# Kernel tuning notes

Hardware: AMD Instinct MI355X
Metric: run time of the kernel (lower is better)

## Reference

```python
import jax, jax.numpy as jnp
import numpy as np

N = 100_000      # nodes
E = 800_000      # edges
NF = 32          # node_feature_size
EF = 32          # edge_feature_size
L = 64           # layer_size
ENTRY = NF + EF          # 64, input width of node_mlp_1
SECOND = NF + L          # 96, input width of node_mlp_2
SLOPE = 0.1              # leakiness
EPS = 1e-5               # BatchNorm1d eps


def _bn(h, g, b):
    # BatchNorm1d in training mode: batch mean, biased variance
    m = h.mean(0)
    v = ((h - m) ** 2).mean(0)
    return (h - m) * jax.lax.rsqrt(v + EPS) * g + b


def _lrelu(h):
    return jnp.where(h > 0, h, SLOPE * h)


def setup_inputs() -> dict:
    key = jax.random.key(0)
    ks = jax.random.split(key, 16)

    def w(k, i, o):
        return (jax.random.normal(k, (i, o), jnp.float32) / np.float32(np.sqrt(i)))

    def bvec(k, o):
        return jax.random.normal(k, (o,), jnp.float32) * 0.01

    inp = {
        "x": jax.random.normal(ks[0], (N, NF), jnp.float32),
        "edge_index": jax.random.randint(ks[1], (2, E), 0, N),
        "edge_attr": jax.random.normal(ks[2], (E, EF), jnp.float32),
        "u": jax.random.normal(ks[3], (1, 4), jnp.float32),
        "batch": jnp.zeros((N,), jnp.int32),
        # node_mlp_1 params
        "m1_g1": jnp.ones((ENTRY,), jnp.float32), "m1_b1": jnp.zeros((ENTRY,), jnp.float32),
        "m1_w1": w(ks[4], ENTRY, L), "m1_c1": bvec(ks[5], L),
        "m1_g2": jnp.ones((L,), jnp.float32), "m1_b2": jnp.zeros((L,), jnp.float32),
        "m1_w2": w(ks[6], L, L), "m1_c2": bvec(ks[7], L),
        "m1_g3": jnp.ones((L,), jnp.float32), "m1_b3": jnp.zeros((L,), jnp.float32),
        "m1_w3": w(ks[8], L, L), "m1_c3": bvec(ks[9], L),
        # node_mlp_2 params
        "m2_g1": jnp.ones((SECOND,), jnp.float32), "m2_b1": jnp.zeros((SECOND,), jnp.float32),
        "m2_w1": w(ks[10], SECOND, SECOND), "m2_c1": bvec(ks[11], SECOND),
        "m2_g2": jnp.ones((SECOND,), jnp.float32), "m2_b2": jnp.zeros((SECOND,), jnp.float32),
        "m2_w2": w(ks[12], SECOND, SECOND), "m2_c2": bvec(ks[13], SECOND),
        "m2_g3": jnp.ones((SECOND,), jnp.float32), "m2_b3": jnp.zeros((SECOND,), jnp.float32),
        "m2_w3": w(ks[14], SECOND, NF), "m2_c3": bvec(ks[15], NF),
    }
    return inp


def reference(x, edge_index, edge_attr, u, batch,
              m1_g1, m1_b1, m1_w1, m1_c1,
              m1_g2, m1_b2, m1_w2, m1_c2,
              m1_g3, m1_b3, m1_w3, m1_c3,
              m2_g1, m2_b1, m2_w1, m2_c1,
              m2_g2, m2_b2, m2_w2, m2_c2,
              m2_g3, m2_b3, m2_w3, m2_c3):
    row, col = edge_index[0], edge_index[1]
    # gather source node features, concat with edge features  [E, ENTRY]
    h = jnp.concatenate([x[row], edge_attr], axis=1)
    # node_mlp_1: BN -> Linear -> LReLU -> BN -> Linear -> LReLU -> BN -> Linear
    h = _lrelu(_bn(h, m1_g1, m1_b1) @ m1_w1 + m1_c1)
    h = _lrelu(_bn(h, m1_g2, m1_b2) @ m1_w2 + m1_c2)
    h = _bn(h, m1_g3, m1_b3) @ m1_w3 + m1_c3
    # scatter-sum back to destination nodes  [N, L]
    agg = jax.ops.segment_sum(h, col, num_segments=x.shape[0])
    # node_mlp_2 on [x, agg]  [N, SECOND]
    h2 = jnp.concatenate([x, agg], axis=1)
    h2 = _lrelu(_bn(h2, m2_g1, m2_b1) @ m2_w1 + m2_c1)
    h2 = _lrelu(_bn(h2, m2_g2, m2_b2) @ m2_w2 + m2_c2)
    out = _bn(h2, m2_g3, m2_b3) @ m2_w3 + m2_c3  # [N, NF]
    return out
```

## Files before the change

kernel.cpp:

```cpp
#include <hip/hip_runtime.h>


typedef unsigned short u16;
typedef __bf16  bf16x8  __attribute__((ext_vector_type(8)));
typedef float   floatx4 __attribute__((ext_vector_type(4)));

#define NBIN 8

__device__ __forceinline__ float bf2f(u16 u) {
  union { float f; unsigned int i; } v; v.i = ((unsigned int)u) << 16; return v.f;
}
__device__ __forceinline__ u16 f2bf(float f) {
  union { float f; unsigned int i; } v; v.f = f;
  unsigned int x = v.i;
  return (u16)((x + 0x7fffu + ((x >> 16) & 1u)) >> 16);
}
__device__ __forceinline__ bf16x8 ldb8(const u16* p) {
  return *reinterpret_cast<const bf16x8*>(p);
}
__device__ __forceinline__ floatx4 mfma16(bf16x8 a, bf16x8 b, floatx4 c) {
  return __builtin_amdgcn_mfma_f32_16x16x32_bf16(a, b, c, 0, 0, 0);
}
__device__ __forceinline__ float loadf(const void* p, long idx, int mode) {
  return mode ? bf2f(((const u16*)p)[idx]) : ((const float*)p)[idx];
}
__device__ __forceinline__ bf16x8 load8(const void* p, long idx, int mode) {
  if (mode) return ldb8((const u16*)p + idx);
  const float* f = (const float*)p + idx;
  bf16x8 r;
#pragma unroll
  for (int j = 0; j < 8; j++) r[j] = (__bf16)f[j];
  return r;
}

__global__ void detect_kernel(const u16* __restrict__ x, int* __restrict__ modep) {
  __shared__ int cnt;
  if (threadIdx.x == 0) cnt = 0;
  __syncthreads();
  int weird = 0;
  for (int i = threadIdx.x; i < 1024; i += blockDim.x) {
    unsigned e = (x[i] >> 7) & 0xFFu;
    if (e == 0xFFu || e >= 0x90u || (e != 0u && e < 0x60u)) weird++;
  }
  atomicAdd(&cnt, weird);
  __syncthreads();
  if (threadIdx.x == 0) *modep = (cnt > 128) ? 0 : 1;
}

__global__ void count_kernel(const int* __restrict__ col, int E,
                             int* __restrict__ deg) {
  for (int e = blockIdx.x * blockDim.x + threadIdx.x; e < E;
       e += gridDim.x * blockDim.x)
    atomicAdd(&deg[col[e]], 1);
}

__global__ void scan1_kernel(const int* __restrict__ deg, int n,
                             int* __restrict__ excl, int* __restrict__ bsum) {
  __shared__ int tmp[2][1024];
  const int tid = threadIdx.x;
  const int i = blockIdx.x * 1024 + tid;
  int v = (i < n) ? deg[i] : 0;
  tmp[0][tid] = v;
  __syncthreads();
  int src = 0;
  for (int off = 1; off < 1024; off <<= 1) {
    int t = tmp[src][tid];
    if (tid >= off) t += tmp[src][tid - off];
    tmp[1 - src][tid] = t;
    src = 1 - src;
    __syncthreads();
  }
  if (i < n) excl[i] = tmp[src][tid] - v;
  if (tid == 1023) bsum[blockIdx.x] = tmp[src][1023];
}

__global__ void scan2_kernel(int* __restrict__ bsum, int nb,
                             int* __restrict__ offsets, int N, int E) {
  if (threadIdx.x == 0) {
    int run = 0;
    for (int i = 0; i < nb; i++) { int v = bsum[i]; bsum[i] = run; run += v; }
    offsets[N] = E;
  }
}

__global__ void scan3_kernel(int* __restrict__ offsets, const int* __restrict__ bsum,
                             int n, int* __restrict__ cursor) {
  int i = blockIdx.x * 1024 + threadIdx.x;
  if (i < n) {
    int v = offsets[i] + bsum[blockIdx.x];
    offsets[i] = v;
    cursor[i] = v;
  }
}

__global__ void scatter_kernel(const int* __restrict__ col, int E,
                               int* __restrict__ cursor, int* __restrict__ perm) {
  for (int e = blockIdx.x * blockDim.x + threadIdx.x; e < E;
       e += gridDim.x * blockDim.x) {
    int d = col[e];
    int pos = atomicAdd(&cursor[d], 1);
    perm[pos] = e;
  }
}

__global__ __launch_bounds__(256) void aggsum_kernel(
    const u16* __restrict__ h_e, const int* __restrict__ perm,
    const int* __restrict__ offsets, float* __restrict__ s_e, int N) {
  const int lane = threadIdx.x & 63, wave = threadIdx.x >> 6;
  for (long n = (long)blockIdx.x * 4 + wave; n < N; n += (long)gridDim.x * 4) {
    int start = offsets[n], end = offsets[n + 1];
    float acc = 0.f;
    for (int j = start; j < end; j++) {
      long e = perm[j];
      acc += bf2f(h_e[e * 64 + lane]);
    }
    s_e[n * 64 + lane] = acc;
  }
}

__global__ void stats0_kernel(const void* __restrict__ x, const void* __restrict__ ea,
                              const int* __restrict__ erow, int E,
                              float* __restrict__ stats, const int* __restrict__ modep) {
  const int mode = *modep;
  const int c = threadIdx.x & 63, es = threadIdx.x >> 6;
  float s = 0.f, q = 0.f;
  for (long e = (long)blockIdx.x * 4 + es; e < E; e += (long)gridDim.x * 4) {
    float v;
    if (c < 32) { int src = erow[e]; v = loadf(x, (long)src * 32 + c, mode); }
    else        { v = loadf(ea, e * 32 + (c - 32), mode); }
    s += v; q += v * v;
  }
  __shared__ float sm1[256], sm2[256];
  sm1[threadIdx.x] = s; sm2[threadIdx.x] = q;
  __syncthreads();
  if (es == 0) {
    for (int i = 1; i < 4; i++) { s += sm1[i * 64 + c]; q += sm2[i * 64 + c]; }
    float* o = stats + (blockIdx.x & (NBIN - 1)) * 128;
    atomicAdd(o + c, s); atomicAdd(o + 64 + c, q);
  }
}

__global__ void statsX_kernel(const void* __restrict__ x, int N,
                              float* __restrict__ stats,
                              const int* __restrict__ modep) {
  const int mode = *modep;
  const int c = threadIdx.x & 31, rs = threadIdx.x >> 5;
  float s = 0.f, q = 0.f;
  for (long r = (long)blockIdx.x * 8 + rs; r < N; r += (long)gridDim.x * 8) {
    float v = loadf(x, r * 32 + c, mode);
    s += v; q += v * v;
  }
  __shared__ float sm1[256], sm2[256];
  sm1[threadIdx.x] = s; sm2[threadIdx.x] = q;
  __syncthreads();
  if (rs == 0) {
    for (int i = 1; i < 8; i++) { s += sm1[i * 32 + c]; q += sm2[i * 32 + c]; }
    float* o = stats + (blockIdx.x & (NBIN - 1)) * 192;
    atomicAdd(o + c, s); atomicAdd(o + 96 + c, q);
  }
}

__global__ void fold_kernel(const float* __restrict__ stats, float inv_rows,
                            const void* __restrict__ g, const void* __restrict__ b,
                            const void* __restrict__ W, const void* __restrict__ c,
                            int K, int OUT,
                            u16* __restrict__ Wpack, float* __restrict__ biasOut,
                            const int* __restrict__ modep) {
  const int mode = *modep;
  __shared__ float s_s[96], s_off[96];
  const int tid = threadIdx.x;
  if (tid < K) {
    float sum = 0.f, sq = 0.f;
    for (int p = 0; p < NBIN; p++) {
      sum += stats[p * 2 * K + tid];
      sq  += stats[p * 2 * K + K + tid];
    }
    float m   = sum * inv_rows;
    float var = sq * inv_rows - m * m;
    float s   = loadf(g, tid, mode) * rsqrtf(var + 1e-5f);
    s_s[tid]  = s;
    s_off[tid] = loadf(b, tid, mode) - m * s;
  }
  __syncthreads();
  for (int n = tid; n < OUT; n += blockDim.x) {
    float acc = loadf(c, n, mode);
    for (int k = 0; k < K; k++) acc += s_off[k] * loadf(W, k * OUT + n, mode);
    biasOut[n] = acc;
  }
  const int H = K / 32, T = OUT / 16;
  const int total = T * H * 64 * 8;
  for (int i = tid; i < total; i += blockDim.x) {
    int j = i & 7, lane = (i >> 3) & 63, th = i >> 9;
    int h = th % H, t = th / H;
    int k = h * 32 + (lane >> 4) * 8 + j;
    int n = t * 16 + (lane & 15);
    Wpack[i] = f2bf(s_s[k] * loadf(W, k * OUT + n, mode));
  }
}


__global__ __launch_bounds__(256) void gemm1_kernel(
    const void* __restrict__ x, const void* __restrict__ ea,
    const int* __restrict__ erow, const u16* __restrict__ Wp,
    const float* __restrict__ bias, u16* __restrict__ hout, int E,
    float* __restrict__ statsOut, const int* __restrict__ modep) {
  const int mode = *modep;
  const int lane = threadIdx.x & 63, wave = threadIdx.x >> 6;
  const int q = lane >> 4, r = lane & 15;
  const long wbase = (long)blockIdx.x * 256 + wave * 64;
  bf16x8 bfr[4][2];
#pragma unroll
  for (int t = 0; t < 4; t++)
#pragma unroll
    for (int h = 0; h < 2; h++)
      bfr[t][h] = ldb8(Wp + ((t * 2 + h) * 64 + lane) * 8);
  float bv[4];
#pragma unroll
  for (int t = 0; t < 4; t++) bv[t] = bias[t * 16 + r];
  float s_[4] = {0, 0, 0, 0}, q_[4] = {0, 0, 0, 0};
#pragma unroll
  for (int r4 = 0; r4 < 4; r4++) {
    const long row0 = wbase + r4 * 16;
    long e = row0 + r; if (e > E - 1) e = E - 1;
    int src = erow[e];
    bf16x8 a0 = load8(x, (long)src * 32 + q * 8, mode);
    bf16x8 a1 = load8(ea, e * 32 + q * 8, mode);
    floatx4 acc[4];
#pragma unroll
    for (int t = 0; t < 4; t++) {
      acc[t] = (floatx4){bv[t], bv[t], bv[t], bv[t]};
      acc[t] = mfma16(a0, bfr[t][0], acc[t]);
      acc[t] = mfma16(a1, bfr[t][1], acc[t]);
    }
#pragma unroll
    for (int t = 0; t < 4; t++)
#pragma unroll
      for (int gi = 0; gi < 4; gi++) {
        long row = row0 + q * 4 + gi;
        if (row < E) {
          float v = acc[t][gi];
          v = v > 0.f ? v : 0.1f * v;
          u16 st = f2bf(v);
          hout[row * 64 + t * 16 + r] = st;
          float vv = bf2f(st);
          s_[t] += vv; q_[t] += vv * vv;
        }
      }
  }
  __shared__ float sm[512];
#pragma unroll
  for (int t = 0; t < 4; t++) {
    float s = s_[t], qq = q_[t];
    s  += __shfl_xor(s, 16, 64);  s  += __shfl_xor(s, 32, 64);
    qq += __shfl_xor(qq, 16, 64); qq += __shfl_xor(qq, 32, 64);
    if (lane < 16) { sm[wave * 128 + t * 16 + lane] = s; sm[wave * 128 + 64 + t * 16 + lane] = qq; }
  }
  __syncthreads();
  if (threadIdx.x < 128) {
    int which = threadIdx.x >> 6, c = threadIdx.x & 63;
    float v = 0.f;
    for (int w = 0; w < 4; w++) v += sm[w * 128 + which * 64 + c];
    atomicAdd(statsOut + (blockIdx.x & (NBIN - 1)) * 128 + which * 64 + c, v);
  }
}

__global__ __launch_bounds__(256) void gemm2_kernel(
    const u16* __restrict__ hin, const u16* __restrict__ Wp,
    const float* __restrict__ bias, u16* __restrict__ hout, int E,
    float* __restrict__ statsOut) {
  const int lane = threadIdx.x & 63, wave = threadIdx.x >> 6;
  const int q = lane >> 4, r = lane & 15;
  const long wbase = (long)blockIdx.x * 256 + wave * 64;
  bf16x8 bfr[4][2];
#pragma unroll
  for (int t = 0; t < 4; t++)
#pragma unroll
    for (int h = 0; h < 2; h++)
      bfr[t][h] = ldb8(Wp + ((t * 2 + h) * 64 + lane) * 8);
  float bv[4];
#pragma unroll
  for (int t = 0; t < 4; t++) bv[t] = bias[t * 16 + r];
  float s_[4] = {0, 0, 0, 0}, q_[4] = {0, 0, 0, 0};
#pragma unroll
  for (int r4 = 0; r4 < 4; r4++) {
    const long row0 = wbase + r4 * 16;
    long e = row0 + r; if (e > E - 1) e = E - 1;
    bf16x8 a0 = ldb8(hin + e * 64 + q * 8);
    bf16x8 a1 = ldb8(hin + e * 64 + 32 + q * 8);
    floatx4 acc[4];
#pragma unroll
    for (int t = 0; t < 4; t++) {
      acc[t] = (floatx4){bv[t], bv[t], bv[t], bv[t]};
      acc[t] = mfma16(a0, bfr[t][0], acc[t]);
      acc[t] = mfma16(a1, bfr[t][1], acc[t]);
    }
#pragma unroll
    for (int t = 0; t < 4; t++)
#pragma unroll
      for (int gi = 0; gi < 4; gi++) {
        long row = row0 + q * 4 + gi;
        if (row < E) {
          float v = acc[t][gi];
          v = v > 0.f ? v : 0.1f * v;
          u16 st = f2bf(v);
          hout[row * 64 + t * 16 + r] = st;
          float vv = bf2f(st);
          s_[t] += vv; q_[t] += vv * vv;
        }
      }
  }
  __shared__ float sm[512];
#pragma unroll
  for (int t = 0; t < 4; t++) {
    float s = s_[t], qq = q_[t];
    s  += __shfl_xor(s, 16, 64);  s  += __shfl_xor(s, 32, 64);
    qq += __shfl_xor(qq, 16, 64); qq += __shfl_xor(qq, 32, 64);
    if (lane < 16) { sm[wave * 128 + t * 16 + lane] = s; sm[wave * 128 + 64 + t * 16 + lane] = qq; }
  }
  __syncthreads();
  if (threadIdx.x < 128) {
    int which = threadIdx.x >> 6, c = threadIdx.x & 63;
    float v = 0.f;
    for (int w = 0; w < 4; w++) v += sm[w * 128 + which * 64 + c];
    atomicAdd(statsOut + (blockIdx.x & (NBIN - 1)) * 128 + which * 64 + c, v);
  }
}

__global__ __launch_bounds__(256) void gemmAgg_kernel(
    const float* __restrict__ s_e, const int* __restrict__ deg,
    const u16* __restrict__ Wp, const float* __restrict__ bias,
    float* __restrict__ agg, int N, float* __restrict__ statsOut) {
  const int lane = threadIdx.x & 63, wave = threadIdx.x >> 6;
  const int q = lane >> 4, r = lane & 15;
  const long wbase = (long)blockIdx.x * 256 + wave * 64;
  bf16x8 bfr[4][2];
#pragma unroll
  for (int t = 0; t < 4; t++)
#pragma unroll
    for (int h = 0; h < 2; h++)
      bfr[t][h] = ldb8(Wp + ((t * 2 + h) * 64 + lane) * 8);
  float bv[4];
#pragma unroll
  for (int t = 0; t < 4; t++) bv[t] = bias[t * 16 + r];
  float s_[4] = {0, 0, 0, 0}, q_[4] = {0, 0, 0, 0};
#pragma unroll
  for (int r4 = 0; r4 < 4; r4++) {
    const long row0 = wbase + r4 * 16;
    long m = row0 + r;
    long mm = m < N ? m : (long)N - 1;
    bf16x8 a0, a1;
    {
      const float* ap = s_e + mm * 64 + q * 8;
#pragma unroll
      for (int j = 0; j < 8; j++) a0[j] = (__bf16)ap[j];
#pragma unroll
      for (int j = 0; j < 8; j++) a1[j] = (__bf16)ap[32 + j];
    }
    floatx4 acc[4];
#pragma unroll
    for (int t = 0; t < 4; t++) {
      acc[t] = (floatx4){0.f, 0.f, 0.f, 0.f};
      acc[t] = mfma16(a0, bfr[t][0], acc[t]);
      acc[t] = mfma16(a1, bfr[t][1], acc[t]);
    }
#pragma unroll
    for (int gi = 0; gi < 4; gi++) {
      long row = row0 + q * 4 + gi;
      if (row < N) {
        float d = (float)deg[row];
#pragma unroll
        for (int t = 0; t < 4; t++) {
          float v = acc[t][gi] + d * bv[t];
          agg[row * 64 + t * 16 + r] = v;
          s_[t] += v; q_[t] += v * v;
        }
      }
    }
  }
  __shared__ float sm[512];
#pragma unroll
  for (int t = 0; t < 4; t++) {
    float s = s_[t], qq = q_[t];
    s  += __shfl_xor(s, 16, 64);  s  += __shfl_xor(s, 32, 64);
    qq += __shfl_xor(qq, 16, 64); qq += __shfl_xor(qq, 32, 64);
    if (lane < 16) { sm[wave * 128 + t * 16 + lane] = s; sm[wave * 128 + 64 + t * 16 + lane] = qq; }
  }
  __syncthreads();
  if (threadIdx.x < 128) {
    int which = threadIdx.x >> 6, c = threadIdx.x & 63;
    float v = 0.f;
    for (int w = 0; w < 4; w++) v += sm[w * 128 + which * 64 + c];
    atomicAdd(statsOut + (blockIdx.x & (NBIN - 1)) * 192 + which * 96 + 32 + c, v);
  }
}


__global__ __launch_bounds__(256) void gemmB1_kernel(
    const void* __restrict__ x, const float* __restrict__ agg,
    const u16* __restrict__ Wp, const float* __restrict__ bias,
    u16* __restrict__ hout, int N, float* __restrict__ statsOut,
    const int* __restrict__ modep) {
  const int mode = *modep;
  const int lane = threadIdx.x & 63, wave = threadIdx.x >> 6;
  const int q = lane >> 4, r = lane & 15;
  const long wbase = (long)blockIdx.x * 256 + wave * 64;
  bf16x8 bfr[6][3];
#pragma unroll
  for (int t = 0; t < 6; t++)
#pragma unroll
    for (int h = 0; h < 3; h++)
      bfr[t][h] = ldb8(Wp + ((t * 3 + h) * 64 + lane) * 8);
  float bv[6];
#pragma unroll
  for (int t = 0; t < 6; t++) bv[t] = bias[t * 16 + r];
  float s_[6] = {0, 0, 0, 0, 0, 0}, q_[6] = {0, 0, 0, 0, 0, 0};
#pragma unroll
  for (int r4 = 0; r4 < 4; r4++) {
    const long row0 = wbase + r4 * 16;
    long m = row0 + r;
    long mm = m < N ? m : (long)N - 1;
    bf16x8 a0 = load8(x, mm * 32 + q * 8, mode);
    bf16x8 a1, a2;
    {
      const float* ap = agg + mm * 64 + q * 8;
#pragma unroll
      for (int j = 0; j < 8; j++) a1[j] = (__bf16)ap[j];
#pragma unroll
      for (int j = 0; j < 8; j++) a2[j] = (__bf16)ap[32 + j];
    }
    floatx4 acc[6];
#pragma unroll
    for (int t = 0; t < 6; t++) {
      acc[t] = (floatx4){bv[t], bv[t], bv[t], bv[t]};
      acc[t] = mfma16(a0, bfr[t][0], acc[t]);
      acc[t] = mfma16(a1, bfr[t][1], acc[t]);
      acc[t] = mfma16(a2, bfr[t][2], acc[t]);
    }
#pragma unroll
    for (int t = 0; t < 6; t++)
#pragma unroll
      for (int gi = 0; gi < 4; gi++) {
        long row = row0 + q * 4 + gi;
        if (row < N) {
          float v = acc[t][gi];
          v = v > 0.f ? v : 0.1f * v;
          u16 st = f2bf(v);
          hout[row * 96 + t * 16 + r] = st;
          float vv = bf2f(st);
          s_[t] += vv; q_[t] += vv * vv;
        }
      }
  }
  __shared__ float sm[768];
#pragma unroll
  for (int t = 0; t < 6; t++) {
    float s = s_[t], qq = q_[t];
    s  += __shfl_xor(s, 16, 64);  s  += __shfl_xor(s, 32, 64);
    qq += __shfl_xor(qq, 16, 64); qq += __shfl_xor(qq, 32, 64);
    if (lane < 16) { sm[wave * 192 + t * 16 + lane] = s; sm[wave * 192 + 96 + t * 16 + lane] = qq; }
  }
  __syncthreads();
  if (threadIdx.x < 192) {
    int which = threadIdx.x / 96, c = threadIdx.x % 96;
    float v = 0.f;
    for (int w = 0; w < 4; w++) v += sm[w * 192 + which * 96 + c];
    atomicAdd(statsOut + (blockIdx.x & (NBIN - 1)) * 192 + which * 96 + c, v);
  }
}

__global__ __launch_bounds__(256) void gemmB2_kernel(
    const u16* __restrict__ hin, const u16* __restrict__ Wp,
    const float* __restrict__ bias, u16* __restrict__ hout, int N,
    float* __restrict__ statsOut) {
  const int lane = threadIdx.x & 63, wave = threadIdx.x >> 6;
  const int q = lane >> 4, r = lane & 15;
  const long wbase = (long)blockIdx.x * 256 + wave * 64;
  bf16x8 bfr[6][3];
#pragma unroll
  for (int t = 0; t < 6; t++)
#pragma unroll
    for (int h = 0; h < 3; h++)
      bfr[t][h] = ldb8(Wp + ((t * 3 + h) * 64 + lane) * 8);
  float bv[6];
#pragma unroll
  for (int t = 0; t < 6; t++) bv[t] = bias[t * 16 + r];
  float s_[6] = {0, 0, 0, 0, 0, 0}, q_[6] = {0, 0, 0, 0, 0, 0};
#pragma unroll
  for (int r4 = 0; r4 < 4; r4++) {
    const long row0 = wbase + r4 * 16;
    long m = row0 + r;
    long mm = m < N ? m : (long)N - 1;
    bf16x8 a0 = ldb8(hin + mm * 96 + q * 8);
    bf16x8 a1 = ldb8(hin + mm * 96 + 32 + q * 8);
    bf16x8 a2 = ldb8(hin + mm * 96 + 64 + q * 8);
    floatx4 acc[6];
#pragma unroll
    for (int t = 0; t < 6; t++) {
      acc[t] = (floatx4){bv[t], bv[t], bv[t], bv[t]};
      acc[t] = mfma16(a0, bfr[t][0], acc[t]);
      acc[t] = mfma16(a1, bfr[t][1], acc[t]);
      acc[t] = mfma16(a2, bfr[t][2], acc[t]);
    }
#pragma unroll
    for (int t = 0; t < 6; t++)
#pragma unroll
      for (int gi = 0; gi < 4; gi++) {
        long row = row0 + q * 4 + gi;
        if (row < N) {
          float v = acc[t][gi];
          v = v > 0.f ? v : 0.1f * v;
          u16 st = f2bf(v);
          hout[row * 96 + t * 16 + r] = st;
          float vv = bf2f(st);
          s_[t] += vv; q_[t] += vv * vv;
        }
      }
  }
  __shared__ float sm[768];
#pragma unroll
  for (int t = 0; t < 6; t++) {
    float s = s_[t], qq = q_[t];
    s  += __shfl_xor(s, 16, 64);  s  += __shfl_xor(s, 32, 64);
    qq += __shfl_xor(qq, 16, 64); qq += __shfl_xor(qq, 32, 64);
    if (lane < 16) { sm[wave * 192 + t * 16 + lane] = s; sm[wave * 192 + 96 + t * 16 + lane] = qq; }
  }
  __syncthreads();
  if (threadIdx.x < 192) {
    int which = threadIdx.x / 96, c = threadIdx.x % 96;
    float v = 0.f;
    for (int w = 0; w < 4; w++) v += sm[w * 192 + which * 96 + c];
    atomicAdd(statsOut + (blockIdx.x & (NBIN - 1)) * 192 + which * 96 + c, v);
  }
}

__global__ __launch_bounds__(256) void gemmB3_kernel(
    const u16* __restrict__ hin, const u16* __restrict__ Wp,
    const float* __restrict__ bias, void* __restrict__ outv, int N,
    const int* __restrict__ modep) {
  const int mode = *modep;
  const int lane = threadIdx.x & 63, wave = threadIdx.x >> 6;
  const int q = lane >> 4, r = lane & 15;
  const long wbase = (long)blockIdx.x * 256 + wave * 64;
  bf16x8 bfr[2][3];
#pragma unroll
  for (int t = 0; t < 2; t++)
#pragma unroll
    for (int h = 0; h < 3; h++)
      bfr[t][h] = ldb8(Wp + ((t * 3 + h) * 64 + lane) * 8);
  float bv[2];
#pragma unroll
  for (int t = 0; t < 2; t++) bv[t] = bias[t * 16 + r];
#pragma unroll
  for (int r4 = 0; r4 < 4; r4++) {
    const long row0 = wbase + r4 * 16;
    long m = row0 + r;
    long mm = m < N ? m : (long)N - 1;
    bf16x8 a0 = ldb8(hin + mm * 96 + q * 8);
    bf16x8 a1 = ldb8(hin + mm * 96 + 32 + q * 8);
    bf16x8 a2 = ldb8(hin + mm * 96 + 64 + q * 8);
    floatx4 acc[2];
#pragma unroll
    for (int t = 0; t < 2; t++) {
      acc[t] = (floatx4){bv[t], bv[t], bv[t], bv[t]};
      acc[t] = mfma16(a0, bfr[t][0], acc[t]);
      acc[t] = mfma16(a1, bfr[t][1], acc[t]);
      acc[t] = mfma16(a2, bfr[t][2], acc[t]);
    }
#pragma unroll
    for (int t = 0; t < 2; t++)
#pragma unroll
      for (int gi = 0; gi < 4; gi++) {
        long row = row0 + q * 4 + gi;
        if (row < N) {
          float v = acc[t][gi];
          if (mode) ((u16*)outv)[row * 32 + t * 16 + r] = f2bf(v);
          else      ((float*)outv)[row * 32 + t * 16 + r] = v;
        }
      }
  }
}

extern "C" void kernel_launch(void* const* d_in, const int* in_sizes, int n_in,
                              void* d_out, int out_size, void* d_ws,
                              size_t ws_size, hipStream_t stream) {
  const int N = in_sizes[0] / 32;
  const int E = in_sizes[2] / 32;

  const void* x    = d_in[0];
  const int*  eidx = (const int*)d_in[1];
  const void* ea   = d_in[2];
  const void *m1_g1 = d_in[5],  *m1_b1 = d_in[6];
  const void *m1_w1 = d_in[7],  *m1_c1 = d_in[8];
  const void *m1_g2 = d_in[9],  *m1_b2 = d_in[10];
  const void *m1_w2 = d_in[11], *m1_c2 = d_in[12];
  const void *m1_g3 = d_in[13], *m1_b3 = d_in[14];
  const void *m1_w3 = d_in[15], *m1_c3 = d_in[16];
  const void *m2_g1 = d_in[17], *m2_b1 = d_in[18];
  const void *m2_w1 = d_in[19], *m2_c1 = d_in[20];
  const void *m2_g2 = d_in[21], *m2_b2 = d_in[22];
  const void *m2_w2 = d_in[23], *m2_c2 = d_in[24];
  const void *m2_g3 = d_in[25], *m2_b3 = d_in[26];
  const void *m2_w3 = d_in[27], *m2_c3 = d_in[28];

  char* w = (char*)d_ws;
  int*   modep  = (int*)w;   w += 16;
  u16*   h_e    = (u16*)w;   w += (size_t)E * 64 * 2;
  u16*   h2b    = (u16*)w;   w += (size_t)N * 96 * 2;
  float* agg    = (float*)w; w += (size_t)N * 64 * 4;
  float* s_e    = (float*)w; w += (size_t)N * 64 * 4;
  int*   offs   = (int*)w;   w += ((size_t)N + 4) * 4;
  int*   cursor = (int*)w;   w += ((size_t)N + 4) * 4;
  int*   perm   = (int*)w;   w += (size_t)E * 4;
  int*   bsum   = (int*)w;   w += 1024 * 4;
  int*   deg    = (int*)w;   w += (size_t)N * 4;
  float* stats0 = (float*)w; w += NBIN * 128 * 4;
  float* stats1 = (float*)w; w += NBIN * 128 * 4;
  float* stats2 = (float*)w; w += NBIN * 128 * 4;
  float* statsB0= (float*)w; w += NBIN * 192 * 4;
  float* statsB1= (float*)w; w += NBIN * 192 * 4;
  float* statsB2= (float*)w; w += NBIN * 192 * 4;
  const size_t zero_bytes = (size_t)N * 4 + NBIN * (128 * 3 + 192 * 3) * 4;
  u16*   Wp1    = (u16*)w;   w += 4096 * 2;
  float* bias1  = (float*)w; w += 64 * 4;
  u16*   Wp2    = (u16*)w;   w += 4096 * 2;
  float* bias2  = (float*)w; w += 64 * 4;
  u16*   Wp3    = (u16*)w;   w += 4096 * 2;
  float* bias3  = (float*)w; w += 64 * 4;
  u16*   WpB1   = (u16*)w;   w += 9216 * 2;
  float* biasB1 = (float*)w; w += 96 * 4;
  u16*   WpB2   = (u16*)w;   w += 9216 * 2;
  float* biasB2 = (float*)w; w += 96 * 4;
  u16*   WpB3   = (u16*)w;   w += 3072 * 2;
  float* biasB3 = (float*)w; w += 32 * 4;

  const int* ecol = eidx + E;
  const float invE = 1.0f / (float)E, invN = 1.0f / (float)N;
  const int gA = (E + 255) / 256, gB = (N + 255) / 256;
  const int nb = (N + 1023) / 1024;

  detect_kernel<<<1, 256, 0, stream>>>((const u16*)x, modep);
  hipMemsetAsync(deg, 0, zero_bytes, stream);

  count_kernel<<<1024, 256, 0, stream>>>(ecol, E, deg);
  scan1_kernel<<<nb, 1024, 0, stream>>>(deg, N, offs, bsum);
  scan2_kernel<<<1, 64, 0, stream>>>(bsum, nb, offs, N, E);
  scan3_kernel<<<nb, 1024, 0, stream>>>(offs, bsum, N, cursor);
  scatter_kernel<<<1024, 256, 0, stream>>>(ecol, E, cursor, perm);
  statsX_kernel<<<512, 256, 0, stream>>>(x, N, statsB0, modep);

  stats0_kernel<<<1024, 256, 0, stream>>>(x, ea, eidx, E, stats0, modep);
  fold_kernel<<<1, 256, 0, stream>>>(stats0, invE, m1_g1, m1_b1, m1_w1, m1_c1,
                                     64, 64, Wp1, bias1, modep);
  gemm1_kernel<<<gA, 256, 0, stream>>>(x, ea, eidx, Wp1, bias1, h_e, E,
                                       stats1, modep);
  fold_kernel<<<1, 256, 0, stream>>>(stats1, invE, m1_g2, m1_b2, m1_w2, m1_c2,
                                     64, 64, Wp2, bias2, modep);
  gemm2_kernel<<<gA, 256, 0, stream>>>(h_e, Wp2, bias2, h_e, E, stats2);

  aggsum_kernel<<<1024, 256, 0, stream>>>(h_e, perm, offs, s_e, N);
  fold_kernel<<<1, 256, 0, stream>>>(stats2, invE, m1_g3, m1_b3, m1_w3, m1_c3,
                                     64, 64, Wp3, bias3, modep);
  gemmAgg_kernel<<<gB, 256, 0, stream>>>(s_e, deg, Wp3, bias3, agg, N, statsB0);

  fold_kernel<<<1, 256, 0, stream>>>(statsB0, invN, m2_g1, m2_b1, m2_w1, m2_c1,
                                     96, 96, WpB1, biasB1, modep);
  gemmB1_kernel<<<gB, 256, 0, stream>>>(x, agg, WpB1, biasB1, h2b, N,
                                        statsB1, modep);
  fold_kernel<<<1, 256, 0, stream>>>(statsB1, invN, m2_g2, m2_b2, m2_w2, m2_c2,
                                     96, 96, WpB2, biasB2, modep);
  gemmB2_kernel<<<gB, 256, 0, stream>>>(h2b, WpB2, biasB2, h2b, N, statsB2);
  fold_kernel<<<1, 256, 0, stream>>>(statsB2, invN, m2_g3, m2_b3, m2_w3, m2_c3,
                                     96, 32, WpB3, biasB3, modep);
  gemmB3_kernel<<<gB, 256, 0, stream>>>(h2b, WpB3, biasB3, d_out, N, modep);
}
```

Baseline: 859.6 us.

## Store edge activations in destination-sorted order and compute gathered-x stats via out-degree weights

The first-layer GEMM now writes each edge's activation row directly into its CSR-sorted slot (via an inverse position array), so gemm2 and the segment-sum read contiguous rows instead of gathering through a permutation. The first BatchNorm's statistics for the gathered x columns are computed algebraically as out-degree-weighted node sums, and the edge-attribute statistics use a separate vectorised kernel. This replaces an E-sized random gather of x with an N-sized pass plus an extra atomic count. The cost is scattered writes in gemm1 and an additional out-degree histogram.

```diff
diff --git a/kernel.cpp b/kernel.cpp
--- a/kernel.cpp
+++ b/kernel.cpp
@@ -47,11 +47,13 @@
   if (threadIdx.x == 0) *modep = (cnt > 128) ? 0 : 1;
 }
 
-__global__ void count_kernel(const int* __restrict__ col, int E,
-                             int* __restrict__ deg) {
+__global__ void count2_kernel(const int* __restrict__ row, const int* __restrict__ col,
+                              int E, int* __restrict__ odeg, int* __restrict__ deg) {
   for (int e = blockIdx.x * blockDim.x + threadIdx.x; e < E;
-       e += gridDim.x * blockDim.x)
+       e += gridDim.x * blockDim.x) {
+    atomicAdd(&odeg[row[e]], 1);
     atomicAdd(&deg[col[e]], 1);
+  }
 }
 
 __global__ void scan1_kernel(const int* __restrict__ deg, int n,
@@ -94,69 +96,96 @@
 }
 
 __global__ void scatter_kernel(const int* __restrict__ col, int E,
-                               int* __restrict__ cursor, int* __restrict__ perm) {
+                               int* __restrict__ cursor, int* __restrict__ ipos) {
   for (int e = blockIdx.x * blockDim.x + threadIdx.x; e < E;
        e += gridDim.x * blockDim.x) {
     int d = col[e];
-    int pos = atomicAdd(&cursor[d], 1);
-    perm[pos] = e;
+    ipos[e] = atomicAdd(&cursor[d], 1);
+  }
+}
+
+__global__ void statsXW_kernel(const void* __restrict__ x, const int* __restrict__ odeg,
+                               int N, float* __restrict__ stats0,
+                               float* __restrict__ statsB0,
+                               const int* __restrict__ modep) {
+  const int mode = *modep;
+  const int c = threadIdx.x & 31, rs = threadIdx.x >> 5;
+  float s = 0.f, q = 0.f, ws = 0.f, wq = 0.f;
+  for (long r = (long)blockIdx.x * 8 + rs; r < N; r += (long)gridDim.x * 8) {
+    float v = loadf(x, r * 32 + c, mode);
+    float w = (float)odeg[r];
+    s += v; q += v * v;
+    ws += w * v; wq += w * v * v;
+  }
+  __shared__ float sm[4][256];
+  sm[0][threadIdx.x] = s; sm[1][threadIdx.x] = q;
+  sm[2][threadIdx.x] = ws; sm[3][threadIdx.x] = wq;
+  __syncthreads();
+  if (threadIdx.x < 32) {
+    for (int i = 1; i < 8; i++) {
+      s  += sm[0][i * 32 + c]; q  += sm[1][i * 32 + c];
+      ws += sm[2][i * 32 + c]; wq += sm[3][i * 32 + c];
+    }
+    const int bin = blockIdx.x & (NBIN - 1);
+    atomicAdd(statsB0 + bin * 192 + c, s);
+    atomicAdd(statsB0 + bin * 192 + 96 + c, q);
+    atomicAdd(stats0 + bin * 128 + c, ws);
+    atomicAdd(stats0 + bin * 128 + 64 + c, wq);
+  }
+}
+
+__global__ void statsEA_kernel(const void* __restrict__ ea, int E,
+                               float* __restrict__ stats,
+                               const int* __restrict__ modep) {
+  const int mode = *modep;
+  const int cg = threadIdx.x & 3;
+  const int rsub = threadIdx.x >> 2;
+  float s[8], q[8];
+#pragma unroll
+  for (int j = 0; j < 8; j++) { s[j] = 0.f; q[j] = 0.f; }
+  for (long r = (long)blockIdx.x * 64 + rsub; r < E; r += (long)gridDim.x * 64) {
+    if (mode) {
+      bf16x8 v = ldb8((const u16*)ea + r * 32 + cg * 8);
+#pragma unroll
+      for (int j = 0; j < 8; j++) { float f = (float)v[j]; s[j] += f; q[j] += f * f; }
+    } else {
+      const float* p = (const float*)ea + r * 32 + cg * 8;
+      float4 a = *(const float4*)p;
+      float4 b = *(const float4*)(p + 4);
+      float f0[8] = {a.x, a.y, a.z, a.w, b.x, b.y, b.z, b.w};
+#pragma unroll
+      for (int j = 0; j < 8; j++) { s[j] += f0[j]; q[j] += f0[j] * f0[j]; }
+    }
+  }
+  const int lane = threadIdx.x & 63;
+#pragma unroll
+  for (int st = 4; st < 64; st <<= 1) {
+#pragma unroll
+    for (int j = 0; j < 8; j++) {
+      s[j] += __shfl_xor(s[j], st, 64);
+      q[j] += __shfl_xor(q[j], st, 64);
+    }
+  }
+  if (lane < 4) {
+    float* o = stats + (blockIdx.x & (NBIN - 1)) * 128;
+#pragma unroll
+    for (int j = 0; j < 8; j++) {
+      atomicAdd(o + 32 + lane * 8 + j, s[j]);
+      atomicAdd(o + 96 + lane * 8 + j, q[j]);
+    }
   }
 }
 
 __global__ __launch_bounds__(256) void aggsum_kernel(
-    const u16* __restrict__ h_e, const int* __restrict__ perm,
-    const int* __restrict__ offsets, float* __restrict__ s_e, int N) {
+    const u16* __restrict__ h_s, const int* __restrict__ offsets,
+    float* __restrict__ s_e, int N) {
   const int lane = threadIdx.x & 63, wave = threadIdx.x >> 6;
   for (long n = (long)blockIdx.x * 4 + wave; n < N; n += (long)gridDim.x * 4) {
     int start = offsets[n], end = offsets[n + 1];
     float acc = 0.f;
-    for (int j = start; j < end; j++) {
-      long e = perm[j];
-      acc += bf2f(h_e[e * 64 + lane]);
-    }
+    for (int j = start; j < end; j++)
+      acc += bf2f(h_s[(long)j * 64 + lane]);
     s_e[n * 64 + lane] = acc;
-  }
-}
-
-__global__ void stats0_kernel(const void* __restrict__ x, const void* __restrict__ ea,
-                              const int* __restrict__ erow, int E,
-                              float* __restrict__ stats, const int* __restrict__ modep) {
-  const int mode = *modep;
-  const int c = threadIdx.x & 63, es = threadIdx.x >> 6;
-  float s = 0.f, q = 0.f;
-  for (long e = (long)blockIdx.x * 4 + es; e < E; e += (long)gridDim.x * 4) {
-    float v;
-    if (c < 32) { int src = erow[e]; v = loadf(x, (long)src * 32 + c, mode); }
-    else        { v = loadf(ea, e * 32 + (c - 32), mode); }
-    s += v; q += v * v;
-  }
-  __shared__ float sm1[256], sm2[256];
-  sm1[threadIdx.x] = s; sm2[threadIdx.x] = q;
-  __syncthreads();
-  if (es == 0) {
-    for (int i = 1; i < 4; i++) { s += sm1[i * 64 + c]; q += sm2[i * 64 + c]; }
-    float* o = stats + (blockIdx.x & (NBIN - 1)) * 128;
-    atomicAdd(o + c, s); atomicAdd(o + 64 + c, q);
-  }
-}
-
-__global__ void statsX_kernel(const void* __restrict__ x, int N,
-                              float* __restrict__ stats,
-                              const int* __restrict__ modep) {
-  const int mode = *modep;
-  const int c = threadIdx.x & 31, rs = threadIdx.x >> 5;
-  float s = 0.f, q = 0.f;
-  for (long r = (long)blockIdx.x * 8 + rs; r < N; r += (long)gridDim.x * 8) {
-    float v = loadf(x, r * 32 + c, mode);
-    s += v; q += v * v;
-  }
-  __shared__ float sm1[256], sm2[256];
-  sm1[threadIdx.x] = s; sm2[threadIdx.x] = q;
-  __syncthreads();
-  if (rs == 0) {
-    for (int i = 1; i < 8; i++) { s += sm1[i * 32 + c]; q += sm2[i * 32 + c]; }
-    float* o = stats + (blockIdx.x & (NBIN - 1)) * 192;
-    atomicAdd(o + c, s); atomicAdd(o + 96 + c, q);
   }
 }
 
@@ -201,8 +230,9 @@
 
 __global__ __launch_bounds__(256) void gemm1_kernel(
     const void* __restrict__ x, const void* __restrict__ ea,
-    const int* __restrict__ erow, const u16* __restrict__ Wp,
-    const float* __restrict__ bias, u16* __restrict__ hout, int E,
+    const int* __restrict__ erow, const int* __restrict__ ipos,
+    const u16* __restrict__ Wp, const float* __restrict__ bias,
+    u16* __restrict__ hout, int E,
     float* __restrict__ statsOut, const int* __restrict__ modep) {
   const int mode = *modep;
   const int lane = threadIdx.x & 63, wave = threadIdx.x >> 6;
@@ -233,19 +263,21 @@
       acc[t] = mfma16(a1, bfr[t][1], acc[t]);
     }
 #pragma unroll
-    for (int t = 0; t < 4; t++)
-#pragma unroll
-      for (int gi = 0; gi < 4; gi++) {
-        long row = row0 + q * 4 + gi;
-        if (row < E) {
+    for (int gi = 0; gi < 4; gi++) {
+      long row = row0 + q * 4 + gi;
+      if (row < E) {
+        long p = ipos[row];
+#pragma unroll
+        for (int t = 0; t < 4; t++) {
           float v = acc[t][gi];
           v = v > 0.f ? v : 0.1f * v;
           u16 st = f2bf(v);
-          hout[row * 64 + t * 16 + r] = st;
+          hout[p * 64 + t * 16 + r] = st;
           float vv = bf2f(st);
           s_[t] += vv; q_[t] += vv * vv;
         }
       }
+    }
   }
   __shared__ float sm[512];
 #pragma unroll
@@ -604,22 +636,23 @@
 
   char* w = (char*)d_ws;
   int*   modep  = (int*)w;   w += 16;
-  u16*   h_e    = (u16*)w;   w += (size_t)E * 64 * 2;
+  u16*   h_s    = (u16*)w;   w += (size_t)E * 64 * 2;
   u16*   h2b    = (u16*)w;   w += (size_t)N * 96 * 2;
   float* agg    = (float*)w; w += (size_t)N * 64 * 4;
   float* s_e    = (float*)w; w += (size_t)N * 64 * 4;
   int*   offs   = (int*)w;   w += ((size_t)N + 4) * 4;
   int*   cursor = (int*)w;   w += ((size_t)N + 4) * 4;
-  int*   perm   = (int*)w;   w += (size_t)E * 4;
+  int*   ipos   = (int*)w;   w += (size_t)E * 4;
   int*   bsum   = (int*)w;   w += 1024 * 4;
   int*   deg    = (int*)w;   w += (size_t)N * 4;
+  int*   odeg   = (int*)w;   w += (size_t)N * 4;
   float* stats0 = (float*)w; w += NBIN * 128 * 4;
   float* stats1 = (float*)w; w += NBIN * 128 * 4;
   float* stats2 = (float*)w; w += NBIN * 128 * 4;
   float* statsB0= (float*)w; w += NBIN * 192 * 4;
   float* statsB1= (float*)w; w += NBIN * 192 * 4;
   float* statsB2= (float*)w; w += NBIN * 192 * 4;
-  const size_t zero_bytes = (size_t)N * 4 + NBIN * (128 * 3 + 192 * 3) * 4;
+  const size_t zero_bytes = (size_t)N * 8 + NBIN * (128 * 3 + 192 * 3) * 4;
   u16*   Wp1    = (u16*)w;   w += 4096 * 2;
   float* bias1  = (float*)w; w += 64 * 4;
   u16*   Wp2    = (u16*)w;   w += 4096 * 2;
@@ -633,6 +666,7 @@
   u16*   WpB3   = (u16*)w;   w += 3072 * 2;
   float* biasB3 = (float*)w; w += 32 * 4;
 
+  const int* erow = eidx;
   const int* ecol = eidx + E;
   const float invE = 1.0f / (float)E, invN = 1.0f / (float)N;
   const int gA = (E + 255) / 256, gB = (N + 255) / 256;
@@ -641,23 +675,24 @@
   detect_kernel<<<1, 256, 0, stream>>>((const u16*)x, modep);
   hipMemsetAsync(deg, 0, zero_bytes, stream);
 
-  count_kernel<<<1024, 256, 0, stream>>>(ecol, E, deg);
+  count2_kernel<<<1024, 256, 0, stream>>>(erow, ecol, E, odeg, deg);
   scan1_kernel<<<nb, 1024, 0, stream>>>(deg, N, offs, bsum);
   scan2_kernel<<<1, 64, 0, stream>>>(bsum, nb, offs, N, E);
   scan3_kernel<<<nb, 1024, 0, stream>>>(offs, bsum, N, cursor);
-  scatter_kernel<<<1024, 256, 0, stream>>>(ecol, E, cursor, perm);
-  statsX_kernel<<<512, 256, 0, stream>>>(x, N, statsB0, modep);
-
-  stats0_kernel<<<1024, 256, 0, stream>>>(x, ea, eidx, E, stats0, modep);
+  scatter_kernel<<<1024, 256, 0, stream>>>(ecol, E, cursor, ipos);
+
+  statsXW_kernel<<<512, 256, 0, stream>>>(x, odeg, N, stats0, statsB0, modep);
+  statsEA_kernel<<<512, 256, 0, stream>>>(ea, E, stats0, modep);
+
   fold_kernel<<<1, 256, 0, stream>>>(stats0, invE, m1_g1, m1_b1, m1_w1, m1_c1,
                                      64, 64, Wp1, bias1, modep);
-  gemm1_kernel<<<gA, 256, 0, stream>>>(x, ea, eidx, Wp1, bias1, h_e, E,
+  gemm1_kernel<<<gA, 256, 0, stream>>>(x, ea, erow, ipos, Wp1, bias1, h_s, E,
                                        stats1, modep);
   fold_kernel<<<1, 256, 0, stream>>>(stats1, invE, m1_g2, m1_b2, m1_w2, m1_c2,
                                      64, 64, Wp2, bias2, modep);
-  gemm2_kernel<<<gA, 256, 0, stream>>>(h_e, Wp2, bias2, h_e, E, stats2);
-
-  aggsum_kernel<<<1024, 256, 0, stream>>>(h_e, perm, offs, s_e, N);
+  gemm2_kernel<<<gA, 256, 0, stream>>>(h_s, Wp2, bias2, h_s, E, stats2);
+
+  aggsum_kernel<<<1024, 256, 0, stream>>>(h_s, offs, s_e, N);
   fold_kernel<<<1, 256, 0, stream>>>(stats2, invE, m1_g3, m1_b3, m1_w3, m1_c3,
                                      64, 64, Wp3, bias3, modep);
   gemmAgg_kernel<<<gB, 256, 0, stream>>>(s_e, deg, Wp3, bias3, agg, N, statsB0);
```

Result: faster. 741.5 us (-13.7%).
